# Kernel optimization log

Measured on AMD Instinct MI355X. Metric: run time of the kernel, lower is better.

## Reference

```python
import jax, jax.numpy as jnp
import numpy as np


def setup_inputs() -> dict:
    key = jax.random.key(0)
    k1, k2, k3, k4, k5 = jax.random.split(key, 5)
    B, S, IN, OUT, R = 4, 2048, 4096, 4096, 16
    x = jax.random.normal(k1, (B, S, IN), dtype=jnp.float32)
    old_weight = jax.random.normal(k2, (OUT, IN), dtype=jnp.float32) * 0.02
    old_bias = jax.random.normal(k3, (OUT,), dtype=jnp.float32) * 0.02
    lora_down = jax.random.normal(k4, (OUT, R), dtype=jnp.float32) * 0.02
    lora_up = jax.random.normal(k5, (R, IN), dtype=jnp.float32) * 0.02
    return {"x": x, "old_weight": old_weight, "old_bias": old_bias,
            "lora_down": lora_down, "lora_up": lora_up}


def reference(x, old_weight, old_bias, lora_down, lora_up):
    # weight = old_weight + lora_down @ lora_up  -> [out, in]
    # output = x @ weight.T + bias               (F.linear)
    weight = old_weight + lora_down @ lora_up
    return jnp.einsum('bsi,oi->bso', x, weight) + old_bias
```

## Files before the change

kernel.cpp:

```cpp
#include <hip/hip_runtime.h>
#include <hip/hip_bf16.h>
#include <stdint.h>


typedef __attribute__((ext_vector_type(4))) float  floatx4;
typedef __attribute__((ext_vector_type(8))) __bf16 bf16x8;

static __device__ __forceinline__ unsigned short f2bf_rne(float f) {
    union { float f; uint32_t u; } v; v.f = f;
    uint32_t r = v.u + 0x7fffu + ((v.u >> 16) & 1u);
    return (unsigned short)(r >> 16);
}

__global__ __launch_bounds__(256) void cvt_x_kernel(const float4* __restrict__ x4,
                                                    uint2* __restrict__ o2,
                                                    int n4) {
    const int stride = gridDim.x * 256;
    for (int i = blockIdx.x * 256 + threadIdx.x; i < n4; i += stride) {
        float4 a = x4[i];
        union { unsigned short s[4]; uint2 v; } o;
        o.s[0] = f2bf_rne(a.x); o.s[1] = f2bf_rne(a.y);
        o.s[2] = f2bf_rne(a.z); o.s[3] = f2bf_rne(a.w);
        o2[i] = o.v;
    }
}

#define MW_ROWS 16
__global__ __launch_bounds__(256) void merge_w_kernel(const float* __restrict__ W,
                                                      const float* __restrict__ down,
                                                      const float* __restrict__ up,
                                                      unsigned short* __restrict__ wb,
                                                      int IN) {
    const int i  = blockIdx.x * 1024 + threadIdx.x * 4;
    const int o0 = blockIdx.y * MW_ROWS;

    float4 u[16];
#pragma unroll
    for (int r = 0; r < 16; r++) u[r] = *(const float4*)(up + r * IN + i);

    for (int o = o0; o < o0 + MW_ROWS; o++) {
        float4 w = *(const float4*)(W + (size_t)o * IN + i);
#pragma unroll
        for (int r = 0; r < 16; r++) {
            const float dr = down[o * 16 + r];
            w.x += dr * u[r].x; w.y += dr * u[r].y;
            w.z += dr * u[r].z; w.w += dr * u[r].w;
        }
        union { unsigned short s[4]; uint2 v; } ov;
        ov.s[0] = f2bf_rne(w.x); ov.s[1] = f2bf_rne(w.y);
        ov.s[2] = f2bf_rne(w.z); ov.s[3] = f2bf_rne(w.w);
        *(uint2*)(wb + (size_t)o * IN + i) = ov.v;
    }
}

#define BM 128
#define BN 128
#define BK 64

static __device__ __forceinline__ void async16(const void* g, void* l) {
    auto* gp = reinterpret_cast<const __attribute__((address_space(1))) uint32_t*>(
        reinterpret_cast<uintptr_t>(g));
    auto* lp = reinterpret_cast<__attribute__((address_space(3))) uint32_t*>(
        reinterpret_cast<uintptr_t>(l));
    __builtin_amdgcn_global_load_lds(gp, lp, 16 , 0, 0);
}

__global__ __launch_bounds__(256) void gemm_bt_bias_kernel(
    const unsigned short* __restrict__ A,
    const unsigned short* __restrict__ B,
    const float* __restrict__ bias,
    float* __restrict__ C,
    int M, int N, int K) {
    __shared__ __align__(16) unsigned short As[BM * BK];
    __shared__ __align__(16) unsigned short Bs[BN * BK];

    const int tid  = threadIdx.x;
    const int wave = tid >> 6;
    const int lane = tid & 63;
    const int wm   = wave >> 1;
    const int wn   = wave & 1;
    const int quad = lane >> 4;
    const int l16  = lane & 15;

    const int tileM = blockIdx.y * BM;
    const int tileN = blockIdx.x * BN;

    const int rowoff = wave * 32 + ((lane >> 3) & 7);
    const int qcol   = ((lane & 7) ^ (lane >> 3)) * 8;
    const unsigned short* aptr = A + (size_t)(tileM + rowoff) * K + qcol;
    const unsigned short* bptr = B + (size_t)(tileN + rowoff) * K + qcol;
    char* abase = (char*)As + wave * 4096;
    char* bbase = (char*)Bs + wave * 4096;

    floatx4 acc[4][4];
#pragma unroll
    for (int i = 0; i < 4; i++)
#pragma unroll
        for (int j = 0; j < 4; j++) acc[i][j] = (floatx4)(0.0f);

    for (int k0 = 0; k0 < K; k0 += BK) {
#pragma unroll
        for (int s = 0; s < 4; s++) {
            async16(aptr + (size_t)s * 8 * K, abase + s * 1024);
            async16(bptr + (size_t)s * 8 * K, bbase + s * 1024);
        }
        aptr += BK; bptr += BK;
        __syncthreads();

#pragma unroll
        for (int h = 0; h < 2; h++) {
            bf16x8 af[4], bfr[4];
#pragma unroll
            for (int t = 0; t < 4; t++) {
                const int arow = wm * 64 + t * 16 + l16;
                const int brow = wn * 64 + t * 16 + l16;
                af[t]  = *(const bf16x8*)((const char*)As + arow * 128 +
                                          (((h * 4 + quad) ^ (l16 & 7)) * 16));
                bfr[t] = *(const bf16x8*)((const char*)Bs + brow * 128 +
                                          (((h * 4 + quad) ^ (l16 & 7)) * 16));
            }
#pragma unroll
            for (int i = 0; i < 4; i++)
#pragma unroll
                for (int j = 0; j < 4; j++)
                    acc[i][j] = __builtin_amdgcn_mfma_f32_16x16x32_bf16(
                        af[i], bfr[j], acc[i][j], 0, 0, 0);
        }
        __syncthreads();
    }

    float bv[4];
#pragma unroll
    for (int j = 0; j < 4; j++) bv[j] = bias[tileN + wn * 64 + j * 16 + l16];

#pragma unroll
    for (int i = 0; i < 4; i++) {
#pragma unroll
        for (int r = 0; r < 4; r++) {
            const int row = tileM + wm * 64 + i * 16 + quad * 4 + r;
            float* crow = C + (size_t)row * N + tileN + wn * 64 + l16;
#pragma unroll
            for (int j = 0; j < 4; j++) crow[j * 16] = acc[i][j][r] + bv[j];
        }
    }
}

extern "C" void kernel_launch(void* const* d_in, const int* in_sizes, int n_in,
                              void* d_out, int out_size, void* d_ws, size_t ws_size,
                              hipStream_t stream) {
    const float* x    = (const float*)d_in[0];
    const float* W    = (const float*)d_in[1];
    const float* bias = (const float*)d_in[2];
    const float* down = (const float*)d_in[3];
    const float* up   = (const float*)d_in[4];
    float* out = (float*)d_out;

    const int IN  = 4096;
    const int OUT = 4096;
    const int M   = in_sizes[0] / IN;

    unsigned short* xb = (unsigned short*)d_ws;
    unsigned short* wb = xb + (size_t)M * IN;

    const int n4 = M * IN / 4;
    cvt_x_kernel<<<n4 / 2 / 256, 256, 0, stream>>>((const float4*)x, (uint2*)xb, n4);
    dim3 mgrid(IN / 1024, OUT / MW_ROWS);
    merge_w_kernel<<<mgrid, 256, 0, stream>>>(W, down, up, wb, IN);

    dim3 grid(OUT / BN, M / BM);
    gemm_bt_bias_kernel<<<grid, 256, 0, stream>>>(xb, wb, bias, out, M, OUT, IN);
}
```

Baseline: 568.5 us.

## Rewrite GEMM as 256x256 tile, 512-thread double-buffered pipelined kernel

Replaces the 128x128 single-buffer GEMM with a 256x256 block tile using 8 waves, 128KB LDS double buffering, and interleaved async global-to-LDS loads of the next K tile during MFMA phases. It adds s_setprio around MFMA bursts, fine-grained barriers with explicit vmcnt waits, and a 1D grid with an XCD-aware block swizzle. The goal is to hide load latency and raise arithmetic intensity per LDS byte. The cost is much higher register and LDS pressure, and the schedule relies on fragile barrier and vmcnt ordering. The prefetch also wraps K indices, so redundant loads happen at the end.

```diff
diff --git a/kernel.cpp b/kernel.cpp
--- a/kernel.cpp
+++ b/kernel.cpp
@@ -53,8 +53,8 @@
     }
 }
 
-#define BM 128
-#define BN 128
+#define BM 256
+#define BN 256
 #define BK 64
 
 static __device__ __forceinline__ void async16(const void* g, void* l) {
@@ -65,82 +65,149 @@
     __builtin_amdgcn_global_load_lds(gp, lp, 16 , 0, 0);
 }
 
-__global__ __launch_bounds__(256) void gemm_bt_bias_kernel(
+__global__ __launch_bounds__(512, 2) void gemm_bt_bias_kernel(
     const unsigned short* __restrict__ A,
     const unsigned short* __restrict__ B,
     const float* __restrict__ bias,
     float* __restrict__ C,
     int M, int N, int K) {
-    __shared__ __align__(16) unsigned short As[BM * BK];
-    __shared__ __align__(16) unsigned short Bs[BN * BK];
+    __shared__ __align__(16) unsigned char smem[131072];
 
     const int tid  = threadIdx.x;
     const int wave = tid >> 6;
     const int lane = tid & 63;
-    const int wm   = wave >> 1;
-    const int wn   = wave & 1;
+    const int wm   = wave >> 2;
+    const int wn   = wave & 3;
     const int quad = lane >> 4;
     const int l16  = lane & 15;
 
-    const int tileM = blockIdx.y * BM;
-    const int tileN = blockIdx.x * BN;
-
-    const int rowoff = wave * 32 + ((lane >> 3) & 7);
-    const int qcol   = ((lane & 7) ^ (lane >> 3)) * 8;
-    const unsigned short* aptr = A + (size_t)(tileM + rowoff) * K + qcol;
-    const unsigned short* bptr = B + (size_t)(tileN + rowoff) * K + qcol;
-    char* abase = (char*)As + wave * 4096;
-    char* bbase = (char*)Bs + wave * 4096;
-
-    floatx4 acc[4][4];
-#pragma unroll
-    for (int i = 0; i < 4; i++)
+    const int nwg = gridDim.x;
+    const int bid = blockIdx.x;
+    const int swz = (bid & 7) * (nwg >> 3) + (bid >> 3);
+    const int ntn = N / BN;
+    const int tileM = (swz / ntn) * BM;
+    const int tileN = (swz % ntn) * BN;
+
+    const int nt = K / BK;
+
+    const int trow = tid >> 3;
+    const int tcol = ((tid & 7) ^ (trow & 7)) << 3;
+    const unsigned short* aG = A + (size_t)(tileM + trow) * K + tcol;
+    const unsigned short* bG = B + (size_t)(tileN + trow) * K + tcol;
+    unsigned char* ldst = smem + tid * 16;
+
+#define STAGE_A(tk, h) do {                                                   \
+        const size_t kof = (size_t)(((tk) & (nt - 1)) * BK);                  \
+        unsigned char* d = ldst + (((tk) & 1) * 32768 + (h) * 16384);         \
+        async16(aG + (size_t)((h) * 128) * K + kof, d);                       \
+        async16(aG + (size_t)((h) * 128 + 64) * K + kof, d + 8192);           \
+    } while (0)
+#define STAGE_B(tk, h) do {                                                   \
+        const size_t kof = (size_t)(((tk) & (nt - 1)) * BK);                  \
+        unsigned char* d = ldst + (65536 + ((tk) & 1) * 32768 + (h) * 16384); \
+        async16(bG + (size_t)((h) * 128) * K + kof, d);                       \
+        async16(bG + (size_t)((h) * 128 + 64) * K + kof, d + 8192);           \
+    } while (0)
+
+    const int qs0 = ((0 * 4 + quad) ^ (l16 & 7)) * 16;
+    const int qs1 = ((1 * 4 + quad) ^ (l16 & 7)) * 16;
+    const int arowb = l16 * 128;
+    const int browb = ((wn & 1) * 64 + l16) * 128;
+
+    floatx4 acc[8][4];
+#pragma unroll
+    for (int i = 0; i < 8; i++)
 #pragma unroll
         for (int j = 0; j < 4; j++) acc[i][j] = (floatx4)(0.0f);
 
-    for (int k0 = 0; k0 < K; k0 += BK) {
-#pragma unroll
-        for (int s = 0; s < 4; s++) {
-            async16(aptr + (size_t)s * 8 * K, abase + s * 1024);
-            async16(bptr + (size_t)s * 8 * K, bbase + s * 1024);
+    STAGE_A(0, 0); STAGE_A(0, 1); STAGE_B(0, 0); STAGE_B(0, 1);
+    STAGE_B(1, 0); STAGE_B(1, 1);
+    asm volatile("s_waitcnt vmcnt(4)" ::: "memory");
+    __builtin_amdgcn_s_barrier();
+
+#define MFMA8(mA, mB)                                                          \
+    _Pragma("unroll")                                                          \
+    for (int n = 0; n < 4; n++) {                                              \
+        acc[mA][n] = __builtin_amdgcn_mfma_f32_16x16x32_bf16(aA0, b0[n], acc[mA][n], 0, 0, 0); \
+        acc[mA][n] = __builtin_amdgcn_mfma_f32_16x16x32_bf16(aA1, b1[n], acc[mA][n], 0, 0, 0); \
+        acc[mB][n] = __builtin_amdgcn_mfma_f32_16x16x32_bf16(aB0, b0[n], acc[mB][n], 0, 0, 0); \
+        acc[mB][n] = __builtin_amdgcn_mfma_f32_16x16x32_bf16(aB1, b1[n], acc[mB][n], 0, 0, 0); \
+    }
+
+#pragma unroll 2
+    for (int kt = 0; kt < nt; ++kt) {
+        const int cur = kt & 1;
+        const unsigned char* Ab = smem + (cur * 32768 + wm * 16384 + arowb);
+        const unsigned char* Bb = smem + (65536 + cur * 32768 + (wn >> 1) * 16384 + browb);
+
+        bf16x8 b0[4], b1[4];
+        bf16x8 aA0, aA1, aB0, aB1;
+
+#pragma unroll
+        for (int n = 0; n < 4; n++) {
+            b0[n] = *(const bf16x8*)(Bb + n * 2048 + qs0);
+            b1[n] = *(const bf16x8*)(Bb + n * 2048 + qs1);
         }
-        aptr += BK; bptr += BK;
-        __syncthreads();
-
-#pragma unroll
-        for (int h = 0; h < 2; h++) {
-            bf16x8 af[4], bfr[4];
-#pragma unroll
-            for (int t = 0; t < 4; t++) {
-                const int arow = wm * 64 + t * 16 + l16;
-                const int brow = wn * 64 + t * 16 + l16;
-                af[t]  = *(const bf16x8*)((const char*)As + arow * 128 +
-                                          (((h * 4 + quad) ^ (l16 & 7)) * 16));
-                bfr[t] = *(const bf16x8*)((const char*)Bs + brow * 128 +
-                                          (((h * 4 + quad) ^ (l16 & 7)) * 16));
-            }
-#pragma unroll
-            for (int i = 0; i < 4; i++)
-#pragma unroll
-                for (int j = 0; j < 4; j++)
-                    acc[i][j] = __builtin_amdgcn_mfma_f32_16x16x32_bf16(
-                        af[i], bfr[j], acc[i][j], 0, 0, 0);
-        }
-        __syncthreads();
-    }
+        aA0 = *(const bf16x8*)(Ab + 0 * 2048 + qs0);
+        aA1 = *(const bf16x8*)(Ab + 0 * 2048 + qs1);
+        aB0 = *(const bf16x8*)(Ab + 1 * 2048 + qs0);
+        aB1 = *(const bf16x8*)(Ab + 1 * 2048 + qs1);
+        STAGE_A(kt + 1, 0);
+        __builtin_amdgcn_s_barrier();
+        __builtin_amdgcn_s_setprio(1);
+        MFMA8(0, 1);
+        __builtin_amdgcn_s_setprio(0);
+        __builtin_amdgcn_s_barrier();
+
+        aA0 = *(const bf16x8*)(Ab + 2 * 2048 + qs0);
+        aA1 = *(const bf16x8*)(Ab + 2 * 2048 + qs1);
+        aB0 = *(const bf16x8*)(Ab + 3 * 2048 + qs0);
+        aB1 = *(const bf16x8*)(Ab + 3 * 2048 + qs1);
+        STAGE_A(kt + 1, 1);
+        __builtin_amdgcn_s_barrier();
+        __builtin_amdgcn_s_setprio(1);
+        MFMA8(2, 3);
+        __builtin_amdgcn_s_setprio(0);
+        __builtin_amdgcn_s_barrier();
+
+        aA0 = *(const bf16x8*)(Ab + 4 * 2048 + qs0);
+        aA1 = *(const bf16x8*)(Ab + 4 * 2048 + qs1);
+        aB0 = *(const bf16x8*)(Ab + 5 * 2048 + qs0);
+        aB1 = *(const bf16x8*)(Ab + 5 * 2048 + qs1);
+        STAGE_B(kt + 2, 0);
+        __builtin_amdgcn_s_barrier();
+        __builtin_amdgcn_s_setprio(1);
+        MFMA8(4, 5);
+        __builtin_amdgcn_s_setprio(0);
+        __builtin_amdgcn_s_barrier();
+
+        aA0 = *(const bf16x8*)(Ab + 6 * 2048 + qs0);
+        aA1 = *(const bf16x8*)(Ab + 6 * 2048 + qs1);
+        aB0 = *(const bf16x8*)(Ab + 7 * 2048 + qs0);
+        aB1 = *(const bf16x8*)(Ab + 7 * 2048 + qs1);
+        STAGE_B(kt + 2, 1);
+        __builtin_amdgcn_s_barrier();
+        __builtin_amdgcn_s_setprio(1);
+        MFMA8(6, 7);
+        __builtin_amdgcn_s_setprio(0);
+        asm volatile("s_waitcnt vmcnt(4)" ::: "memory");
+        __builtin_amdgcn_s_barrier();
+    }
+
+    asm volatile("s_waitcnt vmcnt(0)" ::: "memory");
 
     float bv[4];
 #pragma unroll
-    for (int j = 0; j < 4; j++) bv[j] = bias[tileN + wn * 64 + j * 16 + l16];
-
-#pragma unroll
-    for (int i = 0; i < 4; i++) {
+    for (int n = 0; n < 4; n++) bv[n] = bias[tileN + wn * 64 + n * 16 + l16];
+
+#pragma unroll
+    for (int m = 0; m < 8; m++) {
 #pragma unroll
         for (int r = 0; r < 4; r++) {
-            const int row = tileM + wm * 64 + i * 16 + quad * 4 + r;
+            const int row = tileM + wm * 128 + m * 16 + quad * 4 + r;
             float* crow = C + (size_t)row * N + tileN + wn * 64 + l16;
 #pragma unroll
-            for (int j = 0; j < 4; j++) crow[j * 16] = acc[i][j][r] + bv[j];
+            for (int n = 0; n < 4; n++) crow[n * 16] = acc[m][n][r] + bv[n];
         }
     }
 }
@@ -167,6 +234,6 @@
     dim3 mgrid(IN / 1024, OUT / MW_ROWS);
     merge_w_kernel<<<mgrid, 256, 0, stream>>>(W, down, up, wb, IN);
 
-    dim3 grid(OUT / BN, M / BM);
-    gemm_bt_bias_kernel<<<grid, 256, 0, stream>>>(xb, wb, bias, out, M, OUT, IN);
-}
+    dim3 grid((M / BM) * (OUT / BN));
+    gemm_bt_bias_kernel<<<grid, 512, 0, stream>>>(xb, wb, bias, out, M, OUT, IN);
+}
```

Result: faster. 490.0 us (-13.8%).
